# Performance work log

Measured on AMD Instinct MI355X. Metric: run time of the kernel, lower is better.

Reference implementation:

```python
import jax, jax.numpy as jnp
import numpy as np

EPS = 1e-5
MAG_EPS = 1e-12  # guards sqrt grad at exactly 0


def _conv(x, w, b, pad):
    # x: NCHW, w: OIHW, stride 1, symmetric padding -> SAME for odd kernels
    y = jax.lax.conv_general_dilated(x, w, (1, 1), [(pad, pad), (pad, pad)],
                                     dimension_numbers=('NCHW', 'OIHW', 'NCHW'))
    return y + b[None, :, None, None]


def _cconv(xr, xi, wr, wi, br, bi, pad):
    # apply_complex: (conv_r(xr) - conv_i(xi)) + j(conv_r(xi) + conv_i(xr)), biases inside each real conv
    yr = _conv(xr, wr, br, pad) - _conv(xi, wi, bi, pad)
    yi = _conv(xi, wr, br, pad) + _conv(xr, wi, bi, pad)
    return yr, yi


def _cbn(xr, xi, grr, gri, gii, br, bi):
    # complex batch norm with 2x2 covariance whitening (training-mode batch stats)
    ax = (0, 2, 3)
    bc = lambda v: v[None, :, None, None]
    cr = xr - bc(xr.mean(ax))
    ci = xi - bc(xi.mean(ax))
    Crr = (cr * cr).mean(ax) + EPS
    Cii = (ci * ci).mean(ax) + EPS
    Cri = (cr * ci).mean(ax)
    s = jnp.sqrt(Crr * Cii - Cri * Cri)          # sqrt(det)
    t = jnp.sqrt(Crr + Cii + 2.0 * s)            # sqrt(trace + 2 sqrt(det))
    inv = 1.0 / (s * t)
    Rrr, Rii, Rri = (Cii + s) * inv, (Crr + s) * inv, -Cri * inv
    xhr = bc(Rrr) * cr + bc(Rri) * ci
    xhi = bc(Rri) * cr + bc(Rii) * ci
    yr = bc(grr) * xhr + bc(gri) * xhi + bc(br)
    yi = bc(gri) * xhr + bc(gii) * xhi + bc(bi)
    return yr, yi


def _crelu(xr, xi):
    return jnp.maximum(xr, 0.0), jnp.maximum(xi, 0.0)


def _cmaxpool2(xr, xi):
    # 2x2 max pool selecting the complex value with the largest magnitude
    N, C, H, W = xr.shape
    blk = lambda x: x.reshape(N, C, H // 2, 2, W // 2, 2).transpose(0, 1, 2, 4, 3, 5).reshape(N, C, H // 2, W // 2, 4)
    br_, bi_ = blk(xr), blk(xi)
    idx = jnp.argmax(br_ * br_ + bi_ * bi_, axis=-1, keepdims=True)
    yr = jnp.take_along_axis(br_, idx, axis=-1)[..., 0]
    yi = jnp.take_along_axis(bi_, idx, axis=-1)[..., 0]
    return yr, yi


def _net(x,
         c1_wr, c1_wi, c1_br, c1_bi, b1_grr, b1_gri, b1_gii, b1_br, b1_bi,
         c2_wr, c2_wi, c2_br, c2_bi, b2_grr, b2_gri, b2_gii, b2_br, b2_bi,
         c3_wr, c3_wi, c3_br, c3_bi, b3_grr, b3_gri, b3_gii, b3_br, b3_bi,
         c4_wr, c4_wi, c4_br, c4_bi, b4_grr, b4_gri, b4_gii, b4_br, b4_bi,
         fc1_wr, fc1_wi, fc1_br, fc1_bi, fc2_w, fc2_b):
    # conv1: input has zero imaginary part, so the complex conv folds into two real convs
    xr = _conv(x, c1_wr, c1_br - c1_bi, 5)
    xi = _conv(x, c1_wi, c1_br + c1_bi, 5)
    xr, xi = _cmaxpool2(*_crelu(*_cbn(xr, xi, b1_grr, b1_gri, b1_gii, b1_br, b1_bi)))
    xr, xi = _cconv(xr, xi, c2_wr, c2_wi, c2_br, c2_bi, 2)
    xr, xi = _cmaxpool2(*_crelu(*_cbn(xr, xi, b2_grr, b2_gri, b2_gii, b2_br, b2_bi)))
    xr, xi = _cconv(xr, xi, c3_wr, c3_wi, c3_br, c3_bi, 1)
    xr, xi = _cmaxpool2(*_crelu(*_cbn(xr, xi, b3_grr, b3_gri, b3_gii, b3_br, b3_bi)))
    xr, xi = _cconv(xr, xi, c4_wr, c4_wi, c4_br, c4_bi, 1)
    xr, xi = _cmaxpool2(*_crelu(*_cbn(xr, xi, b4_grr, b4_gri, b4_gii, b4_br, b4_bi)))
    N = xr.shape[0]
    fr, fi = xr.reshape(N, -1), xi.reshape(N, -1)  # (N, 1024)
    er = (fr @ fc1_wr.T + fc1_br) - (fi @ fc1_wi.T + fc1_bi)
    ei = (fi @ fc1_wr.T + fc1_br) + (fr @ fc1_wi.T + fc1_bi)
    er, ei = jnp.maximum(er, 0.0), jnp.maximum(ei, 0.0)  # complex relu
    mag = jnp.sqrt(er * er + ei * ei + MAG_EPS)          # |z|; dropout is identity at eval
    logits = mag @ fc2_w.T + fc2_b
    return logits, er, ei


def setup_inputs() -> dict:
    key = jax.random.key(0)
    ks = iter(jax.random.split(key, 64))
    d = {}
    d['x'] = jax.random.normal(next(ks), (512, 1, 64, 64), jnp.float32)
    for name, cin, cout, k in [('c1', 1, 16, 11), ('c2', 16, 32, 5), ('c3', 32, 64, 3), ('c4', 64, 64, 3)]:
        s = 1.0 / np.sqrt(cin * k * k)
        d[f'{name}_wr'] = jax.random.normal(next(ks), (cout, cin, k, k), jnp.float32) * s
        d[f'{name}_wi'] = jax.random.normal(next(ks), (cout, cin, k, k), jnp.float32) * s
        d[f'{name}_br'] = jax.random.normal(next(ks), (cout,), jnp.float32) * s
        d[f'{name}_bi'] = jax.random.normal(next(ks), (cout,), jnp.float32) * s
    for name, c in [('b1', 16), ('b2', 32), ('b3', 64), ('b4', 64)]:
        d[f'{name}_grr'] = jnp.full((c,), 1.0 / np.sqrt(2.0), jnp.float32)
        d[f'{name}_gri'] = jnp.zeros((c,), jnp.float32)
        d[f'{name}_gii'] = jnp.full((c,), 1.0 / np.sqrt(2.0), jnp.float32)
        d[f'{name}_br'] = jnp.zeros((c,), jnp.float32)
        d[f'{name}_bi'] = jnp.zeros((c,), jnp.float32)
    s = 1.0 / np.sqrt(1024.0)
    d['fc1_wr'] = jax.random.normal(next(ks), (256, 1024), jnp.float32) * s
    d['fc1_wi'] = jax.random.normal(next(ks), (256, 1024), jnp.float32) * s
    d['fc1_br'] = jax.random.normal(next(ks), (256,), jnp.float32) * s
    d['fc1_bi'] = jax.random.normal(next(ks), (256,), jnp.float32) * s
    d['fc2_w'] = jax.random.normal(next(ks), (1000, 256), jnp.float32) * (1.0 / 16.0)
    d['fc2_b'] = jnp.zeros((1000,), jnp.float32)
    return d


def reference(x,
              c1_wr, c1_wi, c1_br, c1_bi, b1_grr, b1_gri, b1_gii, b1_br, b1_bi,
              c2_wr, c2_wi, c2_br, c2_bi, b2_grr, b2_gri, b2_gii, b2_br, b2_bi,
              c3_wr, c3_wi, c3_br, c3_bi, b3_grr, b3_gri, b3_gii, b3_br, b3_bi,
              c4_wr, c4_wi, c4_br, c4_bi, b4_grr, b4_gri, b4_gii, b4_br, b4_bi,
              fc1_wr, fc1_wi, fc1_br, fc1_bi, fc2_w, fc2_b):
    # returns (logits, emb_real, emb_imag); torch returned complex embeddings, split here into real pairs
    return _net(x,
                c1_wr, c1_wi, c1_br, c1_bi, b1_grr, b1_gri, b1_gii, b1_br, b1_bi,
                c2_wr, c2_wi, c2_br, c2_bi, b2_grr, b2_gri, b2_gii, b2_br, b2_bi,
                c3_wr, c3_wi, c3_br, c3_bi, b3_grr, b3_gri, b3_gii, b3_br, b3_bi,
                c4_wr, c4_wi, c4_br, c4_bi, b4_grr, b4_gri, b4_gii, b4_br, b4_bi,
                fc1_wr, fc1_wi, fc1_br, fc1_bi, fc2_w, fc2_b)
```

## Files before the change

### kernel.cpp

```cpp
#include <hip/hip_runtime.h>
#include <math.h>

__global__ __launch_bounds__(256) void fill_kernel(float* p, int n, float v) {
  int i = blockIdx.x * 256 + threadIdx.x;
  if (i < n) p[i] = v;
}

__device__ __forceinline__ void bn_apply_f32(float xr, float xi,
                                             const float* __restrict__ cf,
                                             float grr, float gri, float gii,
                                             float bbr, float bbi, float& yr,
                                             float& yi) {
  float cr = __fsub_rn(xr, cf[0]);
  float ci = __fsub_rn(xi, cf[1]);
  float xhr = __fadd_rn(__fmul_rn(cf[2], cr), __fmul_rn(cf[4], ci));
  float xhi = __fadd_rn(__fmul_rn(cf[4], cr), __fmul_rn(cf[3], ci));
  yr = fmaxf(__fadd_rn(__fadd_rn(__fmul_rn(grr, xhr), __fmul_rn(gri, xhi)), bbr), 0.f);
  yi = fmaxf(__fadd_rn(__fadd_rn(__fmul_rn(gri, xhr), __fmul_rn(gii, xhi)), bbi), 0.f);
}

#define PFMA8(XX, YY, WV1, WV2) \
  XX = fmaf(v4.x, WV1.x, XX);   \
  XX = fmaf(v4.y, WV1.y, XX);   \
  XX = fmaf(v4.z, WV1.z, XX);   \
// ... 52 lines not shown
      float4 wR = swr4[ky * 11 + kx];
      float4 wI = swi4[ky * 11 + kx];
#pragma unroll
      for (int k8 = 0; k8 < 8; ++k8) {
        float v = tb0[k8 * 8];
        a[0][k8] = fmaf(v, wR.x, a[0][k8]);  bb[0][k8] = fmaf(v, wI.x, bb[0][k8]);
        a[1][k8] = fmaf(v, wR.y, a[1][k8]);  bb[1][k8] = fmaf(v, wI.y, bb[1][k8]);
        a[2][k8] = fmaf(v, wR.z, a[2][k8]);  bb[2][k8] = fmaf(v, wI.z, bb[2][k8]);
        a[3][k8] = fmaf(v, wR.w, a[3][k8]);  bb[3][k8] = fmaf(v, wI.w, bb[3][k8]);
      }
#pragma unroll
      for (int k8 = 0; k8 < 8; ++k8) {
        float v = tb1[k8 * 8];
        a[0][8 + k8] = fmaf(v, wR.x, a[0][8 + k8]);  bb[0][8 + k8] = fmaf(v, wI.x, bb[0][8 + k8]);
        a[1][8 + k8] = fmaf(v, wR.y, a[1][8 + k8]);  bb[1][8 + k8] = fmaf(v, wI.y, bb[1][8 + k8]);
        a[2][8 + k8] = fmaf(v, wR.z, a[2][8 + k8]);  bb[2][8 + k8] = fmaf(v, wI.z, bb[2][8 + k8]);
        a[3][8 + k8] = fmaf(v, wR.w, a[3][8 + k8]);  bb[3][8 + k8] = fmaf(v, wI.w, bb[3][8 + k8]);
      }
    }
  }

#pragma unroll
  for (int ci = 0; ci < 4; ++ci) {
    int c = cg * 4 + ci;
    float addR = __fsub_rn(br[c], bi[c]);
    float addI = __fadd_rn(br[c], bi[c]);
    float mr = 0.f, mi = 0.f;
    if (PASS) { mr = coef[c * 5 + 0]; mi = coef[c * 5 + 1]; }
    float a0 = 0.f, a1 = 0.f, a2 = 0.f;
#pragma unroll
    for (int k = 0; k < 16; ++k) {
      float xr = __fadd_rn(a[ci][k], addR);
      float xi = __fadd_rn(bb[ci][k], addI);
      if (PASS == 0) {
        a0 = __fadd_rn(a0, xr);
        a1 = __fadd_rn(a1, xi);
      } else {
        float cr = __fsub_rn(xr, mr), ci2 = __fsub_rn(xi, mi);
        a0 = __fadd_rn(a0, __fmul_rn(cr, cr));
        a1 = __fadd_rn(a1, __fmul_rn(ci2, ci2));
        a2 = __fadd_rn(a2, __fmul_rn(cr, ci2));
      }
    }
    s0[t] = a0; s1[t] = a1; if (PASS) s2[t] = a2;
    __syncthreads();
    if (t < 32) {
      int o = t * 8;
      float v0 = __fadd_rn(__fadd_rn(__fadd_rn(s0[o], s0[o + 1]), __fadd_rn(s0[o + 2], s0[o + 3])),
                           __fadd_rn(__fadd_rn(s0[o + 4], s0[o + 5]), __fadd_rn(s0[o + 6], s0[o + 7])));
      float v1 = __fadd_rn(__fadd_rn(__fadd_rn(s1[o], s1[o + 1]), __fadd_rn(s1[o + 2], s1[o + 3])),
                           __fadd_rn(__fadd_rn(s1[o + 4], s1[o + 5]), __fadd_rn(s1[o + 6], s1[o + 7])));
      float v2 = 0.f;
      if (PASS)
        v2 = __fadd_rn(__fadd_rn(__fadd_rn(s2[o], s2[o + 1]), __fadd_rn(s2[o + 2], s2[o + 3])),
                       __fadd_rn(__fadd_rn(s2[o + 4], s2[o + 5]), __fadd_rn(s2[o + 6], s2[o + 7])));
      s0[t] = v0; s1[t] = v1; if (PASS) s2[t] = v2;
    }
    if (t == 0) {
      for (int wdt = 32; wdt > 1; wdt >>= 1)
        for (int i = 0; i < (wdt >> 1); ++i) {
          s0[i] = __fadd_rn(s0[2 * i], s0[2 * i + 1]);
          s1[i] = __fadd_rn(s1[2 * i], s1[2 * i + 1]);
          if (PASS) s2[i] = __fadd_rn(s2[2 * i], s2[2 * i + 1]);
        }
      constexpr int S = PASS ? 3 : 2;
      size_t base = ((size_t)(n * 16 + c)) * S;
      partial[base + 0] = s0[0];
      partial[base + 1] = s1[0];
      if (PASS) partial[base + 2] = s2[0];
    }
    __syncthreads();
  }
}

__global__ __launch_bounds__(256, 2) void conv1_pool2(
    const float* __restrict__ x, const float* __restrict__ wr,
    const float* __restrict__ wi, const float* __restrict__ br,
    const float* __restrict__ bi, const float* __restrict__ coef,
    const float* __restrict__ grr, const float* __restrict__ gri,
    const float* __restrict__ gii, const float* __restrict__ bbr,
    const float* __restrict__ bbi, float* __restrict__ Pr,
    float* __restrict__ Pi) {
  int b = blockIdx.x;
  int n = b >> 2, cg = b & 3;
  int t = threadIdx.x;
  __shared__ __align__(16) float sx[74 * 84];
  __shared__ __align__(16) float4 swr4[121], swi4[121];

  for (int i = t; i < 74 * 84; i += 256) sx[i] = 0.f;
  for (int idx = t; idx < 484; idx += 256) {
    int wo = idx >> 2, ci = idx & 3;
    ((float*)swr4)[idx] = wr[(size_t)(cg * 4 + ci) * 121 + wo];
    ((float*)swi4)[idx] = wi[(size_t)(cg * 4 + ci) * 121 + wo];
  }
  __syncthreads();
  const float* xn = x + (size_t)n * 4096;
  for (int idx = t; idx < 1024; idx += 256) {
    float4 v = *(const float4*)(xn + idx * 4);
    int iy = idx >> 4, ixb = (idx & 15) * 4;
    int base = C1_ROWBASE(iy + 5) + ixb + 5;
    sx[base + 0] = v.x; sx[base + 1] = v.y;
    sx[base + 2] = v.z; sx[base + 3] = v.w;
  }
  __syncthreads();

  int oyb = t >> 5, ox = t & 31;
  float A[4][16], Bb[4][16];
#pragma unroll
  for (int ci = 0; ci < 4; ++ci)
#pragma unroll
    for (int e = 0; e < 16; ++e) { A[ci][e] = 0.f; Bb[ci][e] = 0.f; }

  for (int ky = 0; ky < 11; ++ky) {
    for (int kx = 0; kx < 11; ++kx) {
      float4 wR = swr4[ky * 11 + kx];
      float4 wI = swi4[ky * 11 + kx];
#pragma unroll
      for (int e = 0; e < 16; ++e) {
        int i = e >> 2, p = e & 3;
        int pr = 2 * (oyb + i * 8) + (p >> 1) + ky;
        int pc = 2 * ox + (p & 1) + kx;
        float v = sx[C1_ROWBASE(pr) + pc];
        A[0][e] = fmaf(v, wR.x, A[0][e]);  Bb[0][e] = fmaf(v, wI.x, Bb[0][e]);
        A[1][e] = fmaf(v, wR.y, A[1][e]);  Bb[1][e] = fmaf(v, wI.y, Bb[1][e]);
        A[2][e] = fmaf(v, wR.z, A[2][e]);  Bb[2][e] = fmaf(v, wI.z, Bb[2][e]);
        A[3][e] = fmaf(v, wR.w, A[3][e]);  Bb[3][e] = fmaf(v, wI.w, Bb[3][e]);
      }
    }
  }

#pragma unroll
  for (int ci = 0; ci < 4; ++ci) {
    int c = cg * 4 + ci;
    float addR = __fsub_rn(br[c], bi[c]);
    float addI = __fadd_rn(br[c], bi[c]);
    const float* cf = coef + c * 5;
    float gR = grr[c], gI = gri[c], gG = gii[c], bR = bbr[c], bI2 = bbi[c];
#pragma unroll
    for (int i = 0; i < 4; ++i) {
      int oy = oyb + i * 8;
      float bestr = 0.f, besti = 0.f, bestm = -1.f;
#pragma unroll
      for (int p = 0; p < 4; ++p) {
        float xr = __fadd_rn(A[ci][i * 4 + p], addR);
        float xi = __fadd_rn(Bb[ci][i * 4 + p], addI);
        float yr, yi;
        bn_apply_f32(xr, xi, cf, gR, gI, gG, bR, bI2, yr, yi);
        float m = __fadd_rn(__fmul_rn(yr, yr), __fmul_rn(yi, yi));
        if (m > bestm) { bestm = m; bestr = yr; besti = yi; }
      }
      size_t o = ((size_t)(n * 16 + c) * 32 + oy) * 32 + ox;
      Pr[o] = bestr;
      Pi[o] = besti;
    }
  }
}

__global__ __launch_bounds__(256) void repack_w(const float* __restrict__ src,
                                                float* __restrict__ dst,
                                                int CIN, int KK, int total) {
  int i = blockIdx.x * 256 + threadIdx.x;
  if (i >= total) return;
  int kk = i % KK;
  int rem = i / KK;
  int ci = rem % CIN;
  int co = rem / CIN;
  dst[((size_t)co * KK + kk) * CIN + ci] = src[i];
}

__global__ __launch_bounds__(256) void transpose_rc(const float* __restrict__ src,
                                                    float* __restrict__ dst,
                                                    int R, int C) {
  int i = blockIdx.x * 256 + threadIdx.x;
  if (i >= R * C) return;
  int r = i / C, c = i % C;
  dst[(size_t)c * R + r] = src[i];
}

#define STAGE_COMP(SRCBASE)                                          \
  {                                                                  \
    const float* src_ = (SRCBASE) + (size_t)n * CIN * HH;            \
    for (int idx = t; idx < RALLOC * H * CINQ; idx += NT) {          \
      int px = idx % (RALLOC * H);                                   \
      int cq = idx / (RALLOC * H);                                   \
      int lr = px / H, col = px - lr * H;                            \
      int gr = r0 + lr;                                              \
      if (gr < 0 || gr >= H) continue;                               \
      const float* sp = src_ + (size_t)cq * 4 * HH + gr * H + col;   \
      float4 v;                                                      \
      v.x = sp[0]; v.y = sp[HH]; v.z = sp[2 * HH]; v.w = sp[3 * HH]; \
      *(float4*)&sin_[(lr * W + col + PAD) * ST1 + cq * 4] = v;      \
    }                                                                \
  }

template <int H, int CIN, int COUT, int K, int PASS>
__global__ __launch_bounds__(COUT * 4, 2) void cconv_band_stats(
    const float* __restrict__ Xr, const float* __restrict__ Xi,
    const float* __restrict__ wrT, const float* __restrict__ wiT,
    const float* __restrict__ br, const float* __restrict__ bi,
    const float* __restrict__ coef, float* __restrict__ partial) {
  constexpr int HH = H * H;
  constexpr int PAD = K / 2, KK = K * K;
  constexpr int CLEN = (HH >= 128) ? 16 : 8;
  constexpr int NLEAF = HH / (8 * CLEN);
  constexpr int BROWS = (CLEN * 8) / H;
  constexpr int RALLOC = BROWS + 2 * PAD;
  constexpr int W = H + 2 * PAD;
  constexpr int ST1 = CIN + 4;
  constexpr int CINQ = CIN / 4;
  constexpr int NT = COUT * 4;
  constexpr int NC = COUT * 8;

  __shared__ __align__(16) float sin_[RALLOC * W * ST1];
  __shared__ float red0[NC], red1[NC], red2[PASS ? NC : 1];

  int b = blockIdx.x;
  int leaf = b % NLEAF;
  int n = b / NLEAF;
  int t = threadIdx.x;
  int r0 = leaf * BROWS - PAD;

  for (int i = t; i < RALLOC * W * ST1; i += NT) sin_[i] = 0.f;
  __syncthreads();
  STAGE_COMP(Xr)
  __syncthreads();

  int c0 = t >> 3, j = t & 7;
  int c1 = c0 + COUT / 2;
  const float* wrb0 = wrT + (size_t)c0 * CIN * KK;
  const float* wib0 = wiT + (size_t)c0 * CIN * KK;
  const float* wrb1 = wrT + (size_t)c1 * CIN * KK;
  const float* wib1 = wiT + (size_t)c1 * CIN * KK;

  float A0[CLEN], D0[CLEN], A1[CLEN], D1[CLEN];
  float B0[CLEN], C0_[CLEN], B1[CLEN], C1_[CLEN];
#pragma unroll
  for (int k = 0; k < CLEN; ++k) {
    A0[k] = 0.f; D0[k] = 0.f; A1[k] = 0.f; D1[k] = 0.f;
    B0[k] = 0.f; C0_[k] = 0.f; B1[k] = 0.f; C1_[k] = 0.f;
  }

#define STATS_TAPS(PH)                                                        \
  for (int ky = 0; ky < K; ++ky) {                                            \
    for (int kx = 0; kx < K; ++kx) {                                          \
      const float* tb = sin_ + (ky * W + kx + j) * ST1;                       \
      const float* wrp0 = wrb0 + (ky * K + kx) * CIN;                         \
      const float* wip0 = wib0 + (ky * K + kx) * CIN;                         \
      const float* wrp1 = wrb1 + (ky * K + kx) * CIN;                         \
      const float* wip1 = wib1 + (ky * K + kx) * CIN;                         \
      _Pragma("unroll 2") for (int cq = 0; cq < CINQ; ++cq) {                 \
        const float* tbc = tb + cq * 4;                                       \
        float4 wR0v = *(const float4*)(wrp0 + cq * 4);                        \
        float4 wI0v = *(const float4*)(wip0 + cq * 4);                        \
        float4 wR1v = *(const float4*)(wrp1 + cq * 4);                        \
        float4 wI1v = *(const float4*)(wip1 + cq * 4);                        \
        _Pragma("unroll") for (int k = 0; k < CLEN; ++k) {                    \
          float4 v4 = *(const float4*)(tbc +                                  \
              (((k * 8) / H) * W + ((k * 8) % H)) * ST1);                     \
          if (PH == 0) {                                                      \
            PFMA8(A0[k], D0[k], wR0v, wI0v)                                   \
            PFMA8(A1[k], D1[k], wR1v, wI1v)                                   \
          } else {                                                            \
            PFMA8(B0[k], C0_[k], wI0v, wR0v)                                  \
            PFMA8(B1[k], C1_[k], wI1v, wR1v)                                  \
          }                                                                   \
        }                                                                     \
      }                                                                       \
    }                                                                         \
  }

  STATS_TAPS(0)
  __syncthreads();
  STAGE_COMP(Xi)
  __syncthreads();
  STATS_TAPS(1)
#undef STATS_TAPS

  {
    float cbR = br[c0], cbI = bi[c0];
    float mr = 0.f, mi = 0.f;
    if (PASS) { mr = coef[c0 * 5 + 0]; mi = coef[c0 * 5 + 1]; }
    float a0 = 0.f, a1 = 0.f, a2 = 0.f;
#pragma unroll
    for (int k = 0; k < CLEN; ++k) {
      float yr = __fsub_rn(__fadd_rn(A0[k], cbR), __fadd_rn(B0[k], cbI));
      float yi = __fadd_rn(__fadd_rn(C0_[k], cbR), __fadd_rn(D0[k], cbI));
      if (PASS == 0) {
        a0 = __fadd_rn(a0, yr);
        a1 = __fadd_rn(a1, yi);
      } else {
        float cr = __fsub_rn(yr, mr), ci = __fsub_rn(yi, mi);
        a0 = __fadd_rn(a0, __fmul_rn(cr, cr));
        a1 = __fadd_rn(a1, __fmul_rn(ci, ci));
        a2 = __fadd_rn(a2, __fmul_rn(cr, ci));
      }
    }
    red0[c0 * 8 + j] = a0; red1[c0 * 8 + j] = a1;
    if (PASS) red2[c0 * 8 + j] = a2;
  }
  {
    float cbR = br[c1], cbI = bi[c1];
    float mr = 0.f, mi = 0.f;
    if (PASS) { mr = coef[c1 * 5 + 0]; mi = coef[c1 * 5 + 1]; }
    float a0 = 0.f, a1 = 0.f, a2 = 0.f;
#pragma unroll
    for (int k = 0; k < CLEN; ++k) {
// ... 328 lines not shown
  for (int ch = 0; ch < 4; ++ch)
#pragma unroll
    for (int k = 0; k < CLT; ++k) {
      A[ch][k] = 0.f; Bq[ch][k] = 0.f; Cc[ch][k] = 0.f; D[ch][k] = 0.f;
    }

#define STORE4_TAPS(PH)                                                       \
  for (int ky = 0; ky < K; ++ky) {                                            \
    for (int kx = 0; kx < K; ++kx) {                                          \
      const float* tb = jbp + (ky * W + kx) * ST1;                            \
      int woff = (ky * K + kx) * CIN;                                         \
      _Pragma("unroll 2") for (int cq = 0; cq < CINQ; ++cq) {                 \
        const float* tbc = tb + cq * 4;                                       \
        float4 wRv[4], wIv[4];                                                \
        _Pragma("unroll") for (int ch = 0; ch < 4; ++ch) {                    \
          wRv[ch] = *(const float4*)(wrb[ch] + woff + cq * 4);                \
          wIv[ch] = *(const float4*)(wib[ch] + woff + cq * 4);                \
        }                                                                     \
        _Pragma("unroll") for (int k = 0; k < CLT; ++k) {                     \
          float4 v4 = *(const float4*)(tbc +                                  \
              (((k * 8) / H) * W + ((k * 8) % H)) * ST1);                     \
          if (PH == 0) {                                                      \
            PFMA8(A[0][k], D[0][k], wRv[0], wIv[0])                           \
            PFMA8(A[1][k], D[1][k], wRv[1], wIv[1])                           \
            PFMA8(A[2][k], D[2][k], wRv[2], wIv[2])                           \
            PFMA8(A[3][k], D[3][k], wRv[3], wIv[3])                           \
          } else {                                                            \
            PFMA8(Bq[0][k], Cc[0][k], wIv[0], wRv[0])                         \
            PFMA8(Bq[1][k], Cc[1][k], wIv[1], wRv[1])                         \
            PFMA8(Bq[2][k], Cc[2][k], wIv[2], wRv[2])                         \
            PFMA8(Bq[3][k], Cc[3][k], wIv[3], wRv[3])                         \
          }                                                                   \
        }                                                                     \
      }                                                                       \
    }                                                                         \
  }

  STORE4_TAPS(0)
  __syncthreads();
  STAGE_COMP(Xi)
  __syncthreads();
  STORE4_TAPS(1)
#undef STORE4_TAPS

#pragma unroll
  for (int ch = 0; ch < 4; ++ch) {
    int c = coff + c0l + ch * CQ;
    float cbR = br[c], cbI = bi[c];
    size_t bbase = ((size_t)n * CG + (c0l + ch * CQ)) * HH;
#pragma unroll
    for (int k = 0; k < CLT; ++k) {
      int px = leaf * CLEN * 8 + (rep * CLT + k) * 8 + j;
      float yr = __fsub_rn(__fadd_rn(A[ch][k], cbR), __fadd_rn(Bq[ch][k], cbI));
      float yi = __fadd_rn(__fadd_rn(Cc[ch][k], cbR), __fadd_rn(D[ch][k], cbI));
      bufR[bbase + px] = yr;
      bufI[bbase + px] = yi;
    }
  }
}

template <int CG, int HH, int CLEN, int PASS>
__global__ __launch_bounds__(CG * 8) void cstats_stream(
    const float* __restrict__ bufR, const float* __restrict__ bufI,
    const float* __restrict__ coef, float* __restrict__ partial, int coff) {
  constexpr int NLEAF = HH / (8 * CLEN);
  constexpr int NT = CG * 8;
  __shared__ float red0[NT], red1[NT], red2[PASS ? NT : 1];
  int b = blockIdx.x;
  int leaf = b % NLEAF;
  int n = b / NLEAF;
  int t = threadIdx.x;
  int cl = t >> 3, j = t & 7;
  int c = coff + cl;
  size_t base = ((size_t)n * CG + cl) * HH + leaf * CLEN * 8 + j;
  float mr = 0.f, mi = 0.f;
  if (PASS) { mr = coef[c * 5 + 0]; mi = coef[c * 5 + 1]; }
  float a0 = 0.f, a1 = 0.f, a2 = 0.f;
#pragma unroll
  for (int k = 0; k < CLEN; ++k) {
    float yr = bufR[base + k * 8];
    float yi = bufI[base + k * 8];
    if (PASS == 0) {
      a0 = __fadd_rn(a0, yr);
      a1 = __fadd_rn(a1, yi);
    } else {
      float cr = __fsub_rn(yr, mr), ci = __fsub_rn(yi, mi);
      a0 = __fadd_rn(a0, __fmul_rn(cr, cr));
      a1 = __fadd_rn(a1, __fmul_rn(ci, ci));
      a2 = __fadd_rn(a2, __fmul_rn(cr, ci));
    }
  }
  red0[t] = a0; red1[t] = a1; if (PASS) red2[t] = a2;
  __syncthreads();
  if (j == 0) {
    constexpr int S = PASS ? 3 : 2;
    int o = cl * 8;
    size_t pb = (((size_t)n * CG + cl) * NLEAF + leaf) * S;
    partial[pb + 0] =
        __fadd_rn(__fadd_rn(__fadd_rn(red0[o], red0[o + 1]), __fadd_rn(red0[o + 2], red0[o + 3])),
                  __fadd_rn(__fadd_rn(red0[o + 4], red0[o + 5]), __fadd_rn(red0[o + 6], red0[o + 7])));
    partial[pb + 1] =
        __fadd_rn(__fadd_rn(__fadd_rn(red1[o], red1[o + 1]), __fadd_rn(red1[o + 2], red1[o + 3])),
                  __fadd_rn(__fadd_rn(red1[o + 4], red1[o + 5]), __fadd_rn(red1[o + 6], red1[o + 7])));
    if (PASS)
      partial[pb + 2] =
          __fadd_rn(__fadd_rn(__fadd_rn(red2[o], red2[o + 1]), __fadd_rn(red2[o + 2], red2[o + 3])),
                    __fadd_rn(__fadd_rn(red2[o + 4], red2[o + 5]), __fadd_rn(red2[o + 6], red2[o + 7])));
  }
}

template <int CG, int H, int COUT>
__global__ __launch_bounds__(256) void cpool_stream(
    const float* __restrict__ bufR, const float* __restrict__ bufI,
    const float* __restrict__ coef, const float* __restrict__ grr,
    const float* __restrict__ gri, const float* __restrict__ gii,
    const float* __restrict__ bbr, const float* __restrict__ bbi,
    float* __restrict__ Pr, float* __restrict__ Pi, int coff) {
  constexpr int OH = H / 2, OHH = OH * OH, HH = H * H;
  int n = blockIdx.x;
  for (int idx = threadIdx.x; idx < CG * OHH; idx += 256) {
    int cl = idx / OHH, q = idx % OHH;
    int oy = q / OH, ox = q % OH;
    int c = coff + cl;
    size_t base = ((size_t)n * CG + cl) * HH;
    const float* cf = coef + c * 5;
    float gR = grr[c], gI = gri[c], gG = gii[c], bR = bbr[c], bI2 = bbi[c];
    float bestr = 0.f, besti = 0.f, bestm = -1.f;
#pragma unroll
    for (int p = 0; p < 4; ++p) {
      size_t o = base + (size_t)(2 * oy + (p >> 1)) * H + 2 * ox + (p & 1);
      float xr = bufR[o], xi = bufI[o];
      float yr, yi;
      bn_apply_f32(xr, xi, cf, gR, gI, gG, bR, bI2, yr, yi);
      float m = __fadd_rn(__fmul_rn(yr, yr), __fmul_rn(yi, yi));
      if (m > bestm) { bestm = m; bestr = yr; besti = yi; }
    }
    size_t o = ((size_t)(n * COUT + c) * OH + oy) * OH + ox;
    Pr[o] = bestr;
    Pi[o] = besti;
  }
}

template <int C, int NLEAF, int TPB>
__global__ __launch_bounds__(TPB) void np_mean_combine3(
    const float* __restrict__ partial, float* __restrict__ coef, float Mf,
    int coff) {
  int t = threadIdx.x;
  if (t >= C * 2) return;
  int c = t >> 1, s = t & 1;
  float acc = 0.f;
  for (int n = 0; n < 512; ++n) {
    const float* p = partial + (((size_t)n * C + c) * NLEAF) * 2 + s;
    float v;
    if (NLEAF == 8)
      v = __fadd_rn(__fadd_rn(__fadd_rn(p[0], p[2]), __fadd_rn(p[4], p[6])),
                    __fadd_rn(__fadd_rn(p[8], p[10]), __fadd_rn(p[12], p[14])));
    else if (NLEAF == 2)
      v = __fadd_rn(p[0], p[2]);
    else
      v = p[0];
    acc = __fadd_rn(acc, v);
  }
  coef[(coff + c) * 5 + s] = __fdiv_rn(acc, Mf);
}

template <int C, int NLEAF, int TPB>
__global__ __launch_bounds__(TPB) void np_cov_combine3(
    const float* __restrict__ partial, float* __restrict__ coef, float Mf,
    int coff) {
  __shared__ float sums[C * 3];
  int t = threadIdx.x;
  if (t < C * 3) {
    int c = t / 3, s = t % 3;
    float acc = 0.f;
    for (int n = 0; n < 512; ++n) {
      const float* p = partial + (((size_t)n * C + c) * NLEAF) * 3 + s;
      float v;
      if (NLEAF == 8)
        v = __fadd_rn(__fadd_rn(__fadd_rn(p[0], p[3]), __fadd_rn(p[6], p[9])),
                      __fadd_rn(__fadd_rn(p[12], p[15]), __fadd_rn(p[18], p[21])));
      else if (NLEAF == 2)
        v = __fadd_rn(p[0], p[3]);
      else
        v = p[0];
      acc = __fadd_rn(acc, v);
    }
    sums[c * 3 + s] = acc;
  }
  __syncthreads();
  if (t < C) {
    float Crr = __fadd_rn(__fdiv_rn(sums[t * 3 + 0], Mf), 1e-5f);
    float Cii = __fadd_rn(__fdiv_rn(sums[t * 3 + 1], Mf), 1e-5f);
    float Cri = __fdiv_rn(sums[t * 3 + 2], Mf);
    float s_ = __fsqrt_rn(__fsub_rn(__fmul_rn(Crr, Cii), __fmul_rn(Cri, Cri)));
    float t_ = __fsqrt_rn(__fadd_rn(__fadd_rn(Crr, Cii), __fmul_rn(2.f, s_)));
    float inv = __fdiv_rn(1.f, __fmul_rn(s_, t_));
    int cg = coff + t;
    coef[cg * 5 + 2] = __fmul_rn(__fadd_rn(Cii, s_), inv);
    coef[cg * 5 + 3] = __fmul_rn(__fadd_rn(Crr, s_), inv);
    coef[cg * 5 + 4] = __fmul_rn(-Cri, inv);
  }
}

__global__ __launch_bounds__(256) void fc_head_kernel(
    const float* __restrict__ Fr, const float* __restrict__ Fi,
    const float* __restrict__ wrT, const float* __restrict__ wiT,
    const float* __restrict__ br, const float* __restrict__ bi,
    const float* __restrict__ w2T, const float* __restrict__ b2,
    float* __restrict__ logits, float* __restrict__ er_out,
    float* __restrict__ ei_out) {
  int n = blockIdx.x, t = threadIdx.x;
  __shared__ float sFr[1024], sFi[1024];
  __shared__ double sMag[256];
  for (int idx = t; idx < 1024; idx += 256) {
    sFr[idx] = Fr[(size_t)n * 1024 + idx];
    sFi[idx] = Fi[(size_t)n * 1024 + idx];
  }
  __syncthreads();
  {
    double er = 0.0, ei = 0.0;
    for (int k = 0; k < 1024; ++k) {
      double fx = (double)sFr[k], fy = (double)sFi[k];
      double a = (double)wrT[(size_t)k * 256 + t];
      double bb = (double)wiT[(size_t)k * 256 + t];
      er += fx * a - fy * bb;
      ei += fy * a + fx * bb;
    }
    double bR = (double)br[t], bI = (double)bi[t];
    er = fmax(er + (bR - bI), 0.0);
    ei = fmax(ei + (bR + bI), 0.0);
    er_out[(size_t)n * 256 + t] = (float)er;
    ei_out[(size_t)n * 256 + t] = (float)ei;
    sMag[t] = sqrt(er * er + ei * ei + 1e-12);
  }
  __syncthreads();
#pragma unroll
  for (int j = 0; j < 4; ++j) {
    int o = j * 256 + t;
    if (o < 1000) {
      double acc = 0.0;
      for (int k = 0; k < 256; ++k)
        acc += sMag[k] * (double)w2T[(size_t)k * 1000 + o];
      logits[(size_t)n * 1000 + o] = (float)(acc + (double)b2[o]);
    }
  }
}

extern "C" void kernel_launch(void* const* d_in, const int* in_sizes, int n_in,
                              void* d_out, int out_size, void* d_ws,
                              size_t ws_size, hipStream_t stream) {
  (void)in_sizes; (void)n_in;
  const float* x = (const float*)d_in[0];
  const float* c1_wr = (const float*)d_in[1];
  const float* c1_wi = (const float*)d_in[2];
  const float* c1_br = (const float*)d_in[3];
  const float* c1_bi = (const float*)d_in[4];
  const float* c2_wr = (const float*)d_in[5];
  const float* c2_wi = (const float*)d_in[6];
  const float* c2_br = (const float*)d_in[7];
  const float* c2_bi = (const float*)d_in[8];
  const float* c3_wr = (const float*)d_in[9];
  const float* c3_wi = (const float*)d_in[10];
  const float* c3_br = (const float*)d_in[11];
  const float* c3_bi = (const float*)d_in[12];
  const float* c4_wr = (const float*)d_in[13];
  const float* c4_wi = (const float*)d_in[14];
  const float* c4_br = (const float*)d_in[15];
  const float* c4_bi = (const float*)d_in[16];
  const float* b1_grr = (const float*)d_in[17];
  const float* b1_gri = (const float*)d_in[18];
  const float* b1_gii = (const float*)d_in[19];
  const float* b1_br = (const float*)d_in[20];
  const float* b1_bi = (const float*)d_in[21];
  const float* b2_grr = (const float*)d_in[22];
  const float* b2_gri = (const float*)d_in[23];
  const float* b2_gii = (const float*)d_in[24];
  const float* b2_br = (const float*)d_in[25];
  const float* b2_bi = (const float*)d_in[26];
  const float* b3_grr = (const float*)d_in[27];
  const float* b3_gri = (const float*)d_in[28];
  const float* b3_gii = (const float*)d_in[29];
  const float* b3_br = (const float*)d_in[30];
  const float* b3_bi = (const float*)d_in[31];
  const float* b4_grr = (const float*)d_in[32];
  const float* b4_gri = (const float*)d_in[33];
  const float* b4_gii = (const float*)d_in[34];
  const float* b4_br = (const float*)d_in[35];
  const float* b4_bi = (const float*)d_in[36];
  const float* fc1_wr = (const float*)d_in[37];
  const float* fc1_wi = (const float*)d_in[38];
  const float* fc1_br = (const float*)d_in[39];
  const float* fc1_bi = (const float*)d_in[40];
  const float* fc2_w = (const float*)d_in[41];
  const float* fc2_b = (const float*)d_in[42];

  float* outL = (float*)d_out;
  float* er = outL + 512 * 1000;
  float* ei = er + 512 * 256;

  const size_t NEED = 101057792;
  const size_t NEED2 = 135005440;
  const size_t NEED3 = 236848384;
  if (ws_size < NEED) {
    fill_kernel<<<(out_size + 255) / 256, 256, 0, stream>>>(
        (float*)d_out, out_size, (float)(ws_size >> 20));
    return;
  }
  const bool big3 = (ws_size >= NEED3);
  const bool big = (ws_size >= NEED2);
  char* w = (char*)d_ws;
  float* P1r = (float*)(w + 0);
  float* P1i = (float*)(w + 33554432);
  float* P2r = (float*)(w + 67108864);
  float* P2i = (float*)(w + 83886080);
  float* P3r = (float*)(w + 0);
  float* P3i = (float*)(w + 8388608);
  float* P4r = (float*)(w + 16777216);
  float* P4i = (float*)(w + 18874368);
  float* partialT = (float*)(w + 100663296);
  float* partial2 = (float*)(w + 67108864);
  float* coef = (float*)(w + 101056512);
  float* c2_wrT = (float*)(w + 100663296);
  float* c2_wiT = (float*)(w + 100663296 + 51200);
  float* c3_wrT = (float*)(w + 100663296);
  float* c3_wiT = (float*)(w + 100663296 + 73728);
  float* c4_wrT = (float*)(w + 20971520);
  float* c4_wiT = (float*)(w + 20971520 + 147456);
  float* fc1_wrT = (float*)(w + 33554432);
  float* fc1_wiT = (float*)(w + 34603008);
  float* fc2_wT = (float*)(w + 35651584);
  float* buf3R = (float*)(w + 16777216);
  float* buf3I = (float*)(w + 33554432);
  float* partial3s = (float*)(w + 50331648);
  float* buf4R = (float*)(w + 67108864);
  float* buf4I = (float*)(w + 75497472);
  float* buf2R = (float*)(w + 101057792);
  float* buf2I = (float*)(w + 117835008);
  float* partial2g = (float*)(w + 134612224);
  float* buf2R3 = (float*)(w + 101057792);
  float* buf2I3 = (float*)(w + 168166656);
  float* partial2g3 = (float*)(w + 235275520);

  conv1_stats2<0><<<2048, 256, 0, stream>>>(x, c1_wr, c1_wi, c1_br, c1_bi,
                                            coef, partialT);
  np_mean_combine3<16, 1, 64><<<1, 64, 0, stream>>>(partialT, coef, 2097152.f, 0);
  conv1_stats2<1><<<2048, 256, 0, stream>>>(x, c1_wr, c1_wi, c1_br, c1_bi,
                                            coef, partialT);
  np_cov_combine3<16, 1, 64><<<1, 64, 0, stream>>>(partialT, coef, 2097152.f, 0);
  conv1_pool2<<<2048, 256, 0, stream>>>(x, c1_wr, c1_wi, c1_br, c1_bi, coef,
                                        b1_grr, b1_gri, b1_gii, b1_br, b1_bi,
                                        P1r, P1i);

  repack_w<<<50, 256, 0, stream>>>(c2_wr, c2_wrT, 16, 25, 12800);
  repack_w<<<50, 256, 0, stream>>>(c2_wi, c2_wiT, 16, 25, 12800);
  if (big3) {
    cconv_band_store<32, 16, 32, 32, 5, 2><<<4096, 256, 0, stream>>>(
        P1r, P1i, c2_wrT, c2_wiT, c2_br, c2_bi, 0, buf2R3, buf2I3);
    cstats_stream<32, 1024, 16, 0><<<4096, 256, 0, stream>>>(
        buf2R3, buf2I3, coef, partial2g3, 0);
    np_mean_combine3<32, 8, 64><<<1, 64, 0, stream>>>(partial2g3, coef,
                                                      524288.f, 0);
    cstats_stream<32, 1024, 16, 1><<<4096, 256, 0, stream>>>(
        buf2R3, buf2I3, coef, partial2g3, 0);
    np_cov_combine3<32, 8, 128><<<1, 128, 0, stream>>>(partial2g3, coef,
                                                       524288.f, 0);
    cpool_stream<32, 32, 32><<<512, 256, 0, stream>>>(
        buf2R3, buf2I3, coef, b2_grr, b2_gri, b2_gii, b2_br, b2_bi, P2r, P2i,
        0);
  } else if (big) {
    for (int g = 0; g < 4; ++g) {
      cconv_band_store<32, 16, 32, 8, 5, 4><<<4096, 128, 0, stream>>>(
          P1r, P1i, c2_wrT, c2_wiT, c2_br, c2_bi, g * 8, buf2R, buf2I);
      cstats_stream<8, 1024, 16, 0><<<4096, 64, 0, stream>>>(
          buf2R, buf2I, coef, partial2g, g * 8);
      np_mean_combine3<8, 8, 64><<<1, 64, 0, stream>>>(partial2g, coef,
                                                       524288.f, g * 8);
      cstats_stream<8, 1024, 16, 1><<<4096, 64, 0, stream>>>(
          buf2R, buf2I, coef, partial2g, g * 8);
      np_cov_combine3<8, 8, 64><<<1, 64, 0, stream>>>(partial2g, coef,
                                                      524288.f, g * 8);
      cpool_stream<8, 32, 32><<<512, 256, 0, stream>>>(
          buf2R, buf2I, coef, b2_grr, b2_gri, b2_gii, b2_br, b2_bi, P2r, P2i,
          g * 8);
    }
  } else {
    cconv_band_stats<32, 16, 32, 5, 0><<<4096, 128, 0, stream>>>(
        P1r, P1i, c2_wrT, c2_wiT, c2_br, c2_bi, coef, partial2);
    np_mean_combine3<32, 8, 64><<<1, 64, 0, stream>>>(partial2, coef,
                                                      524288.f, 0);
    cconv_band_stats<32, 16, 32, 5, 1><<<4096, 128, 0, stream>>>(
        P1r, P1i, c2_wrT, c2_wiT, c2_br, c2_bi, coef, partial2);
    np_cov_combine3<32, 8, 128><<<1, 128, 0, stream>>>(partial2, coef,
                                                       524288.f, 0);
    cconv_band_pool<32, 16, 32, 5, 2><<<4096, 128, 0, stream>>>(
        P1r, P1i, c2_wrT, c2_wiT, c2_br, c2_bi, coef, b2_grr, b2_gri, b2_gii,
        b2_br, b2_bi, P2r, P2i);
  }

  repack_w<<<72, 256, 0, stream>>>(c3_wr, c3_wrT, 32, 9, 18432);
  repack_w<<<72, 256, 0, stream>>>(c3_wi, c3_wiT, 32, 9, 18432);
  for (int g = 0; g < 2; ++g) {
    cconv_band_store4<16, 32, 64, 32, 3, 4><<<1024, 256, 0, stream>>>(
        P2r, P2i, c3_wrT, c3_wiT, c3_br, c3_bi, g * 32, buf3R, buf3I);
    cstats_stream<32, 256, 16, 0><<<1024, 256, 0, stream>>>(
        buf3R, buf3I, coef, partial3s, g * 32);
    np_mean_combine3<32, 2, 64><<<1, 64, 0, stream>>>(partial3s, coef,
                                                      131072.f, g * 32);
    cstats_stream<32, 256, 16, 1><<<1024, 256, 0, stream>>>(
        buf3R, buf3I, coef, partial3s, g * 32);
    np_cov_combine3<32, 2, 128><<<1, 128, 0, stream>>>(partial3s, coef,
                                                       131072.f, g * 32);
    cpool_stream<32, 16, 64><<<512, 256, 0, stream>>>(
        buf3R, buf3I, coef, b3_grr, b3_gri, b3_gii, b3_br, b3_bi, P3r, P3i,
        g * 32);
  }

  repack_w<<<144, 256, 0, stream>>>(c4_wr, c4_wrT, 64, 9, 36864);
  repack_w<<<144, 256, 0, stream>>>(c4_wi, c4_wiT, 64, 9, 36864);
  cconv_band_store4<8, 64, 64, 64, 3, 2><<<512, 256, 0, stream>>>(
      P3r, P3i, c4_wrT, c4_wiT, c4_br, c4_bi, 0, buf4R, buf4I);
  cstats_stream<64, 64, 8, 0><<<512, 512, 0, stream>>>(buf4R, buf4I, coef,
                                                       partialT, 0);
  np_mean_combine3<64, 1, 128><<<1, 128, 0, stream>>>(partialT, coef,
                                                      32768.f, 0);
  cstats_stream<64, 64, 8, 1><<<512, 512, 0, stream>>>(buf4R, buf4I, coef,
                                                       partialT, 0);
  np_cov_combine3<64, 1, 192><<<1, 192, 0, stream>>>(partialT, coef,
                                                     32768.f, 0);
  cpool_stream<64, 8, 64><<<512, 256, 0, stream>>>(
      buf4R, buf4I, coef, b4_grr, b4_gri, b4_gii, b4_br, b4_bi, P4r, P4i, 0);

  transpose_rc<<<1024, 256, 0, stream>>>(fc1_wr, fc1_wrT, 256, 1024);
  transpose_rc<<<1024, 256, 0, stream>>>(fc1_wi, fc1_wiT, 256, 1024);
  transpose_rc<<<1000, 256, 0, stream>>>(fc2_w, fc2_wT, 1000, 256);
  fc_head_kernel<<<512, 256, 0, stream>>>(P4r, P4i, fc1_wrT, fc1_wiT, fc1_br,
                                          fc1_bi, fc2_wT, fc2_b, outL, er, ei);
}
```

Baseline: 2.486 ms.

## Compute conv1 once into a buffer and stream stats and pooling

```diff
diff --git a/kernel.cpp b/kernel.cpp
--- a/kernel.cpp
+++ b/kernel.cpp
@@ -228,6 +228,86 @@
       size_t o = ((size_t)(n * 16 + c) * 32 + oy) * 32 + ox;
       Pr[o] = bestr;
       Pi[o] = besti;
+    }
+  }
+}
+
+__global__ __launch_bounds__(256, 2) void conv1_store(
+    const float* __restrict__ x, const float* __restrict__ wr,
+    const float* __restrict__ wi, const float* __restrict__ br,
+    const float* __restrict__ bi, int cgoff, float* __restrict__ bufR,
+    float* __restrict__ bufI) {
+  int b = blockIdx.x;
+  int n = b >> 1, cgl = b & 1;
+  int cg = cgoff + cgl;
+  int t = threadIdx.x;
+  __shared__ __align__(16) float sx[74 * 84];
+  __shared__ __align__(16) float4 swr4[121], swi4[121];
+
+  for (int i = t; i < 74 * 84; i += 256) sx[i] = 0.f;
+  for (int idx = t; idx < 484; idx += 256) {
+    int wo = idx >> 2, ci = idx & 3;
+    ((float*)swr4)[idx] = wr[(size_t)(cg * 4 + ci) * 121 + wo];
+    ((float*)swi4)[idx] = wi[(size_t)(cg * 4 + ci) * 121 + wo];
+  }
+  __syncthreads();
+  const float* xn = x + (size_t)n * 4096;
+  for (int idx = t; idx < 1024; idx += 256) {
+    float4 v = *(const float4*)(xn + idx * 4);
+    int iy = idx >> 4, ixb = (idx & 15) * 4;
+    int base = C1_ROWBASE(iy + 5) + ixb + 5;
+    sx[base + 0] = v.x; sx[base + 1] = v.y;
+    sx[base + 2] = v.z; sx[base + 3] = v.w;
+  }
+  __syncthreads();
+
+  int leaf = t >> 3, j = t & 7;
+  float a[4][16], bb[4][16];
+#pragma unroll
+  for (int ci = 0; ci < 4; ++ci)
+#pragma unroll
+    for (int k = 0; k < 16; ++k) { a[ci][k] = 0.f; bb[ci][k] = 0.f; }
+
+  for (int ky = 0; ky < 11; ++ky) {
+    int pr0 = leaf * 2 + ky;
+    int base0 = C1_ROWBASE(pr0) + j;
+    int base1 = C1_ROWBASE(pr0 + 1) + j;
+    for (int kx = 0; kx < 11; ++kx) {
+      const float* tb0 = sx + base0 + kx;
+      const float* tb1 = sx + base1 + kx;
+      float4 wR = swr4[ky * 11 + kx];
+      float4 wI = swi4[ky * 11 + kx];
+#pragma unroll
+      for (int k8 = 0; k8 < 8; ++k8) {
+        float v = tb0[k8 * 8];
+        a[0][k8] = fmaf(v, wR.x, a[0][k8]);  bb[0][k8] = fmaf(v, wI.x, bb[0][k8]);
+        a[1][k8] = fmaf(v, wR.y, a[1][k8]);  bb[1][k8] = fmaf(v, wI.y, bb[1][k8]);
+        a[2][k8] = fmaf(v, wR.z, a[2][k8]);  bb[2][k8] = fmaf(v, wI.z, bb[2][k8]);
+        a[3][k8] = fmaf(v, wR.w, a[3][k8]);  bb[3][k8] = fmaf(v, wI.w, bb[3][k8]);
+      }
+#pragma unroll
+      for (int k8 = 0; k8 < 8; ++k8) {
+        float v = tb1[k8 * 8];
+        a[0][8 + k8] = fmaf(v, wR.x, a[0][8 + k8]);  bb[0][8 + k8] = fmaf(v, wI.x, bb[0][8 + k8]);
+        a[1][8 + k8] = fmaf(v, wR.y, a[1][8 + k8]);  bb[1][8 + k8] = fmaf(v, wI.y, bb[1][8 + k8]);
+        a[2][8 + k8] = fmaf(v, wR.z, a[2][8 + k8]);  bb[2][8 + k8] = fmaf(v, wI.z, bb[2][8 + k8]);
+        a[3][8 + k8] = fmaf(v, wR.w, a[3][8 + k8]);  bb[3][8 + k8] = fmaf(v, wI.w, bb[3][8 + k8]);
+      }
+    }
+  }
+
+#pragma unroll
+  for (int ci = 0; ci < 4; ++ci) {
+    int c = cg * 4 + ci;
+    float addR = __fsub_rn(br[c], bi[c]);
+    float addI = __fadd_rn(br[c], bi[c]);
+    int cl = cgl * 4 + ci;
+    size_t base = ((size_t)n * 8 + cl) * 4096;
+#pragma unroll
+    for (int k = 0; k < 16; ++k) {
+      int px = leaf * 128 + k * 8 + j;
+      bufR[base + px] = __fadd_rn(a[ci][k], addR);
+      bufI[base + px] = __fadd_rn(bb[ci][k], addI);
     }
   }
 }
@@ -862,7 +942,16 @@
   for (int n = 0; n < 512; ++n) {
     const float* p = partial + (((size_t)n * C + c) * NLEAF) * 2 + s;
     float v;
-    if (NLEAF == 8)
+    if (NLEAF == 32) {
+      float q[32];
+#pragma unroll
+      for (int i = 0; i < 32; ++i) q[i] = p[i * 2];
+#pragma unroll
+      for (int wd = 32; wd > 1; wd >>= 1)
+#pragma unroll
+        for (int i = 0; i < (wd >> 1); ++i) q[i] = __fadd_rn(q[2 * i], q[2 * i + 1]);
+      v = q[0];
+    } else if (NLEAF == 8)
       v = __fadd_rn(__fadd_rn(__fadd_rn(p[0], p[2]), __fadd_rn(p[4], p[6])),
                     __fadd_rn(__fadd_rn(p[8], p[10]), __fadd_rn(p[12], p[14])));
     else if (NLEAF == 2)
@@ -886,7 +975,16 @@
     for (int n = 0; n < 512; ++n) {
       const float* p = partial + (((size_t)n * C + c) * NLEAF) * 3 + s;
       float v;
-      if (NLEAF == 8)
+      if (NLEAF == 32) {
+        float q[32];
+#pragma unroll
+        for (int i = 0; i < 32; ++i) q[i] = p[i * 3];
+#pragma unroll
+        for (int wd = 32; wd > 1; wd >>= 1)
+#pragma unroll
+          for (int i = 0; i < (wd >> 1); ++i) q[i] = __fadd_rn(q[2 * i], q[2 * i + 1]);
+        v = q[0];
+      } else if (NLEAF == 8)
         v = __fadd_rn(__fadd_rn(__fadd_rn(p[0], p[3]), __fadd_rn(p[6], p[9])),
                       __fadd_rn(__fadd_rn(p[12], p[15]), __fadd_rn(p[18], p[21])));
       else if (NLEAF == 2)
@@ -1050,16 +1148,39 @@
   float* buf2R3 = (float*)(w + 101057792);
   float* buf2I3 = (float*)(w + 168166656);
   float* partial2g3 = (float*)(w + 235275520);
-
-  conv1_stats2<0><<<2048, 256, 0, stream>>>(x, c1_wr, c1_wi, c1_br, c1_bi,
-                                            coef, partialT);
-  np_mean_combine3<16, 1, 64><<<1, 64, 0, stream>>>(partialT, coef, 2097152.f, 0);
-  conv1_stats2<1><<<2048, 256, 0, stream>>>(x, c1_wr, c1_wi, c1_br, c1_bi,
-                                            coef, partialT);
-  np_cov_combine3<16, 1, 64><<<1, 64, 0, stream>>>(partialT, coef, 2097152.f, 0);
-  conv1_pool2<<<2048, 256, 0, stream>>>(x, c1_wr, c1_wi, c1_br, c1_bi, coef,
-                                        b1_grr, b1_gri, b1_gii, b1_br, b1_bi,
-                                        P1r, P1i);
+  float* buf1R = (float*)(w + 101057792);
+  float* buf1I = (float*)(w + 168166656);
+  float* partial1 = (float*)(w + 67108864);
+
+  if (big3) {
+    for (int g = 0; g < 2; ++g) {
+      conv1_store<<<1024, 256, 0, stream>>>(x, c1_wr, c1_wi, c1_br, c1_bi,
+                                            g * 2, buf1R, buf1I);
+      cstats_stream<8, 4096, 16, 0><<<16384, 64, 0, stream>>>(
+          buf1R, buf1I, coef, partial1, g * 8);
+      np_mean_combine3<8, 32, 64><<<1, 64, 0, stream>>>(partial1, coef,
+                                                        2097152.f, g * 8);
+      cstats_stream<8, 4096, 16, 1><<<16384, 64, 0, stream>>>(
+          buf1R, buf1I, coef, partial1, g * 8);
+      np_cov_combine3<8, 32, 64><<<1, 64, 0, stream>>>(partial1, coef,
+                                                       2097152.f, g * 8);
+      cpool_stream<8, 64, 16><<<512, 256, 0, stream>>>(
+          buf1R, buf1I, coef, b1_grr, b1_gri, b1_gii, b1_br, b1_bi, P1r, P1i,
+          g * 8);
+    }
+  } else {
+    conv1_stats2<0><<<2048, 256, 0, stream>>>(x, c1_wr, c1_wi, c1_br, c1_bi,
+                                              coef, partialT);
+    np_mean_combine3<16, 1, 64><<<1, 64, 0, stream>>>(partialT, coef,
+                                                      2097152.f, 0);
+    conv1_stats2<1><<<2048, 256, 0, stream>>>(x, c1_wr, c1_wi, c1_br, c1_bi,
+                                              coef, partialT);
+    np_cov_combine3<16, 1, 64><<<1, 64, 0, stream>>>(partialT, coef,
+                                                     2097152.f, 0);
+    conv1_pool2<<<2048, 256, 0, stream>>>(x, c1_wr, c1_wi, c1_br, c1_bi, coef,
+                                          b1_grr, b1_gri, b1_gii, b1_br,
+                                          b1_bi, P1r, P1i);
+  }
 
   repack_w<<<50, 256, 0, stream>>>(c2_wr, c2_wrT, 16, 25, 12800);
   repack_w<<<50, 256, 0, stream>>>(c2_wi, c2_wiT, 16, 25, 12800);
```

After: 3.022 ms. 21.6% more time.
